# Kernel tuning notes

Hardware: AMD Instinct MI355X
Metric: run time of the kernel (lower is better)

## Reference

```python
import jax, jax.numpy as jnp
import numpy as np

IN_FEATURES = 4096
OUT_FEATURES = 4096
Q_MAX = 127.0  # int8 activation range
EPS = 1e-10


def setup_inputs() -> dict:
    key = jax.random.key(0)
    k1, k2, k3 = jax.random.split(key, 3)
    x = jax.random.normal(k1, (4, 2048, IN_FEATURES), dtype=jnp.float32)
    # Ternary weight in {-1, 0, +1} (the unpacked content of w_packed from pack_tl1).
    w_raw = jax.random.normal(k2, (OUT_FEATURES, IN_FEATURES), dtype=jnp.float32)
    scale = jnp.mean(jnp.abs(w_raw))  # quantize_ternary: scale = |w|.mean()
    w_t = jnp.clip(jnp.round(w_raw / (scale + EPS)), -1.0, 1.0)
    bias = jax.random.normal(k3, (OUT_FEATURES,), dtype=jnp.float32)
    return {"x": x, "w_t": w_t, "w_scale": scale, "bias": bias}


def reference(x, w_t, w_scale, bias):
    """TernaryLinear forward: per-row int8 activation quant, ternary matmul
    with int32 accumulation, scale dequant, bias add.

    x: [..., in], w_t: [out, in] in {-1,0,+1}, w_scale: scalar, bias: [out].
    """
    lead = x.shape[:-1]
    x2 = x.reshape(-1, IN_FEATURES)  # [T, in]
    # Per-row absmax int8 quantization of activations.
    absmax = jnp.max(jnp.abs(x2), axis=-1, keepdims=True)  # [T, 1]
    act_scale = jnp.maximum(absmax, EPS) / Q_MAX
    xq = jnp.clip(jnp.round(x2 / act_scale), -Q_MAX, Q_MAX)  # int-valued [T, in]
    # int32 accumulation (exact in int32; values bounded by 127 * 4096).
    acc = jnp.matmul(xq.astype(jnp.int32), w_t.astype(jnp.int32).T)  # [T, out]
    # Dequantize: y ~= (x @ w_t.T) * w_scale, then bias.
    y = acc.astype(jnp.float32) * act_scale * w_scale + bias
    return y.reshape(*lead, OUT_FEATURES)
```

## Files before the change

kernel.cpp:

```cpp
#include <hip/hip_runtime.h>
#include <stdint.h>

#define T_ROWS 8192
#define IN_F 4096
#define OUT_F 4096

using i32x4 = __attribute__((ext_vector_type(4))) int;
using i32x16 = __attribute__((ext_vector_type(16))) int;

#define GLOBAL_AS __attribute__((address_space(1)))
#define LDS_AS __attribute__((address_space(3)))

static __device__ __forceinline__ void load_lds16(const void* g, void* l) {
    __builtin_amdgcn_global_load_lds((const GLOBAL_AS uint32_t*)g,
                                     (LDS_AS uint32_t*)l, 16, 0, 0);
}

__global__ __launch_bounds__(256) void prep_kernel(const float* __restrict__ x,
                                                   int8_t* __restrict__ xq,
                                                   float* __restrict__ scales,
                                                   const float* __restrict__ w,
                                                   int8_t* __restrict__ w8) {
    if (blockIdx.x < T_ROWS) {
        const int row = blockIdx.x;
        const float* xr = x + (size_t)row * IN_F;
        const float4* xr4 = (const float4*)xr;

        float4 v[4];
        float amax = 0.0f;
#pragma unroll
        for (int i = 0; i < 4; ++i) {
            v[i] = xr4[threadIdx.x + 256 * i];
            amax = fmaxf(amax, fmaxf(fmaxf(fabsf(v[i].x), fabsf(v[i].y)),
                                     fmaxf(fabsf(v[i].z), fabsf(v[i].w))));
        }
#pragma unroll
        for (int off = 32; off; off >>= 1)
            amax = fmaxf(amax, __shfl_xor(amax, off, 64));
        __shared__ float smax[4];
        if ((threadIdx.x & 63) == 0) smax[threadIdx.x >> 6] = amax;
        __syncthreads();
        amax = fmaxf(fmaxf(smax[0], smax[1]), fmaxf(smax[2], smax[3]));

        const float act_scale = fmaxf(amax, 1e-10f) / 127.0f;
        if (threadIdx.x == 0) scales[row] = act_scale;

        int* xqr = (int*)(xq + (size_t)row * IN_F);
#pragma unroll
        for (int i = 0; i < 4; ++i) {
            int q0 = (int)fminf(fmaxf(rintf(v[i].x / act_scale), -127.0f), 127.0f);
            int q1 = (int)fminf(fmaxf(rintf(v[i].y / act_scale), -127.0f), 127.0f);
            int q2 = (int)fminf(fmaxf(rintf(v[i].z / act_scale), -127.0f), 127.0f);
            int q3 = (int)fminf(fmaxf(rintf(v[i].w / act_scale), -127.0f), 127.0f);
            int packed = (q0 & 0xff) | ((q1 & 0xff) << 8) | ((q2 & 0xff) << 16) | (q3 << 24);
            xqr[threadIdx.x + 256 * i] = packed;
        }
    } else {
        const float4* w4 = (const float4*)w;
        int* o4 = (int*)w8;
        size_t base = (size_t)(blockIdx.x - T_ROWS) * 1024 + threadIdx.x;
#pragma unroll
        for (int i = 0; i < 4; ++i) {
            size_t idx = base + 256 * i;
            float4 v = w4[idx];
            int q0 = (int)v.x, q1 = (int)v.y, q2 = (int)v.z, q3 = (int)v.w;
            o4[idx] = (q0 & 0xff) | ((q1 & 0xff) << 8) | ((q2 & 0xff) << 16) | (q3 << 24);
        }
    }
}

__global__ __launch_bounds__(512, 2) void gemm_kernel(const int8_t* __restrict__ xq,
                                                      const int8_t* __restrict__ w8,
                                                      const float* __restrict__ scales,
                                                      const float* __restrict__ bias,
                                                      const float* __restrict__ wscale_p,
                                                      float* __restrict__ out) {
    __shared__ __align__(16) int8_t As[2 * 256 * 128];
    __shared__ __align__(16) int8_t Bs[2 * 256 * 128];

    const int tid = threadIdx.x;
    const int lane = tid & 63;
    const int w = tid >> 6;
    const int wr = w >> 2;
    const int wc = w & 3;
    const int l31 = lane & 31;
    const int lh = lane >> 5;
    const int le = lane & 7;

    int bid = blockIdx.x;
    bid = (bid & 7) * 64 + (bid >> 3);
    const int brow = (bid >> 4) * 256;
    const int bcol = (bid & 15) * 256;

    const int lrow = lane >> 3;
    const int lslot = (lane & 7) ^ lrow;
    const int8_t* srcA = xq + (size_t)(brow + lrow) * IN_F + lslot * 16;
    const int8_t* srcB = w8 + (size_t)(bcol + lrow) * IN_F + lslot * 16;

    const int aBase = (wr * 128 + l31) * 128;
    const int bBase = (wc * 64 + l31) * 128;
    const int slo[4] = { ((0 + lh) ^ le) << 4, ((2 + lh) ^ le) << 4,
                         ((4 + lh) ^ le) << 4, ((6 + lh) ^ le) << 4 };

#define STAGE(LDSA, SRC, BUF, H, KT) do {                                          \
    load_lds16((SRC) + (size_t)((H) * 128 + w * 8) * IN_F + (KT) * 128,            \
               (void*)((LDSA) + (BUF) * 32768 + ((H) * 16 + w) * 1024));           \
    load_lds16((SRC) + (size_t)((H) * 128 + (w + 8) * 8) * IN_F + (KT) * 128,      \
               (void*)((LDSA) + (BUF) * 32768 + ((H) * 16 + w + 8) * 1024));       \
} while (0)

#define PF(FA, FB, BUF, KS) do {                                                   \
    _Pragma("unroll") for (int mi = 0; mi < 4; ++mi)                               \
        FA[mi] = *(const i32x4*)(As + (BUF) * 32768 + aBase + mi * 4096 + slo[KS]);\
    _Pragma("unroll") for (int ni = 0; ni < 2; ++ni)                               \
        FB[ni] = *(const i32x4*)(Bs + (BUF) * 32768 + bBase + ni * 4096 + slo[KS]);\
} while (0)

#define MFMA8(FA, FB) do {                                                         \
    __builtin_amdgcn_s_setprio(1);                                                 \
    _Pragma("unroll") for (int mi = 0; mi < 4; ++mi)                               \
    _Pragma("unroll") for (int ni = 0; ni < 2; ++ni)                               \
        acc[mi][ni] = __builtin_amdgcn_mfma_i32_32x32x32_i8(FA[mi], FB[ni],        \
                                                            acc[mi][ni], 0, 0, 0); \
    __builtin_amdgcn_s_setprio(0);                                                 \
} while (0)

#define BARFENCE do { __builtin_amdgcn_s_barrier(); asm volatile("" ::: "memory"); } while (0)
#define VM0 asm volatile("s_waitcnt vmcnt(0)" ::: "memory")

    i32x16 acc[4][2] = {};
    i32x4 a0[4], b0[2], a1[4], b1[2];

    STAGE(As, srcA, 0, 0, 0);
    STAGE(As, srcA, 0, 1, 0);
    STAGE(Bs, srcB, 0, 0, 0);
    STAGE(Bs, srcB, 0, 1, 0);
    VM0;
    BARFENCE;
    PF(a0, b0, 0, 0);

    for (int t = 0; t < 16; ++t) {
        const int k1 = (2 * t + 1) & 31;
        const int k2 = (2 * t + 2) & 31;
        PF(a1, b1, 0, 1);
        STAGE(As, srcA, 1, 0, k1);
        STAGE(As, srcA, 1, 1, k1);
        STAGE(Bs, srcB, 1, 0, k1);
        MFMA8(a0, b0);
        PF(a0, b0, 0, 2);
        STAGE(Bs, srcB, 1, 1, k1);
        MFMA8(a1, b1);
        PF(a1, b1, 0, 3);
        MFMA8(a0, b0);
        VM0;
        BARFENCE;
        PF(a0, b0, 1, 0);
        MFMA8(a1, b1);
        BARFENCE;
        PF(a1, b1, 1, 1);
        STAGE(As, srcA, 0, 0, k2);
        STAGE(As, srcA, 0, 1, k2);
        STAGE(Bs, srcB, 0, 0, k2);
        MFMA8(a0, b0);
        PF(a0, b0, 1, 2);
        STAGE(Bs, srcB, 0, 1, k2);
        MFMA8(a1, b1);
        PF(a1, b1, 1, 3);
        MFMA8(a0, b0);
        VM0;
        BARFENCE;
        PF(a0, b0, 0, 0);
        MFMA8(a1, b1);
        BARFENCE;
    }

    const float ws = wscale_p[0];
#pragma unroll
    for (int mi = 0; mi < 4; ++mi) {
#pragma unroll
        for (int q = 0; q < 4; ++q) {
#pragma unroll
            for (int r = 0; r < 4; ++r) {
                const int row = brow + wr * 128 + mi * 32 + q * 8 + r + 4 * lh;
                const float sc = scales[row] * ws;
#pragma unroll
                for (int ni = 0; ni < 2; ++ni) {
                    const int col = bcol + wc * 64 + ni * 32 + l31;
                    out[(size_t)row * OUT_F + col] =
                        (float)acc[mi][ni][q * 4 + r] * sc + bias[col];
                }
            }
        }
    }
#undef STAGE
#undef PF
#undef MFMA8
#undef BARFENCE
#undef VM0
}

extern "C" void kernel_launch(void* const* d_in, const int* in_sizes, int n_in,
                              void* d_out, int out_size, void* d_ws, size_t ws_size,
                              hipStream_t stream) {
    const float* x       = (const float*)d_in[0];
    const float* w_t     = (const float*)d_in[1];
    const float* w_scale = (const float*)d_in[2];
    const float* bias    = (const float*)d_in[3];
    float* out = (float*)d_out;

    int8_t* xq     = (int8_t*)d_ws;
    float*  scales = (float*)((char*)d_ws + (size_t)T_ROWS * IN_F);
    int8_t* w8     = (int8_t*)((char*)d_ws + (size_t)T_ROWS * IN_F + T_ROWS * sizeof(float));

    prep_kernel<<<T_ROWS + (OUT_F * IN_F) / (16 * 256), 256, 0, stream>>>(
        x, xq, scales, w_t, w8);

    gemm_kernel<<<(T_ROWS / 256) * (OUT_F / 256), 512, 0, stream>>>(
        xq, w8, scales, bias, w_scale, out);
}
```

Baseline: 192.5 us.

## Add extra LDS swizzle bit and pin LDS-load/MFMA overlap with sched barriers

```diff
diff --git a/kernel.cpp b/kernel.cpp
--- a/kernel.cpp
+++ b/kernel.cpp
@@ -93,7 +93,7 @@
     const int bcol = (bid & 15) * 256;
 
     const int lrow = lane >> 3;
-    const int lslot = (lane & 7) ^ lrow;
+    const int lslot = (lane & 7) ^ lrow ^ (((w >> 2) & 1) << 2);
     const int8_t* srcA = xq + (size_t)(brow + lrow) * IN_F + lslot * 16;
     const int8_t* srcB = w8 + (size_t)(bcol + lrow) * IN_F + lslot * 16;
 
@@ -111,9 +111,11 @@
 
 #define PF(FA, FB, BUF, KS) do {                                                   \
     _Pragma("unroll") for (int mi = 0; mi < 4; ++mi)                               \
-        FA[mi] = *(const i32x4*)(As + (BUF) * 32768 + aBase + mi * 4096 + slo[KS]);\
+        FA[mi] = *(const i32x4*)(As + (BUF) * 32768 + aBase + mi * 4096 +          \
+                                 (slo[KS] ^ ((mi & 1) << 6)));                     \
     _Pragma("unroll") for (int ni = 0; ni < 2; ++ni)                               \
-        FB[ni] = *(const i32x4*)(Bs + (BUF) * 32768 + bBase + ni * 4096 + slo[KS]);\
+        FB[ni] = *(const i32x4*)(Bs + (BUF) * 32768 + bBase + ni * 4096 +          \
+                                 (slo[KS] ^ ((ni & 1) << 6)));                     \
 } while (0)
 
 #define MFMA8(FA, FB) do {                                                         \
@@ -125,6 +127,16 @@
     __builtin_amdgcn_s_setprio(0);                                                 \
 } while (0)
 
+#define PHASE(PFS, STAGES, FA, FB) do {                                            \
+    PFS;                                                                           \
+    STAGES;                                                                        \
+    __builtin_amdgcn_sched_barrier(0);                                             \
+    asm volatile("s_waitcnt lgkmcnt(6)" ::: "memory");                             \
+    __builtin_amdgcn_sched_barrier(0);                                             \
+    MFMA8(FA, FB);                                                                 \
+    __builtin_amdgcn_sched_barrier(0);                                             \
+} while (0)
+
 #define BARFENCE do { __builtin_amdgcn_s_barrier(); asm volatile("" ::: "memory"); } while (0)
 #define VM0 asm volatile("s_waitcnt vmcnt(0)" ::: "memory")
 
@@ -142,35 +154,25 @@
     for (int t = 0; t < 16; ++t) {
         const int k1 = (2 * t + 1) & 31;
         const int k2 = (2 * t + 2) & 31;
-        PF(a1, b1, 0, 1);
-        STAGE(As, srcA, 1, 0, k1);
-        STAGE(As, srcA, 1, 1, k1);
-        STAGE(Bs, srcB, 1, 0, k1);
-        MFMA8(a0, b0);
-        PF(a0, b0, 0, 2);
-        STAGE(Bs, srcB, 1, 1, k1);
-        MFMA8(a1, b1);
-        PF(a1, b1, 0, 3);
-        MFMA8(a0, b0);
+        PHASE(PF(a1, b1, 0, 1),
+              STAGE(As, srcA, 1, 0, k1); STAGE(As, srcA, 1, 1, k1);
+              STAGE(Bs, srcB, 1, 0, k1),
+              a0, b0);
+        PHASE(PF(a0, b0, 0, 2), STAGE(Bs, srcB, 1, 1, k1), a1, b1);
+        PHASE(PF(a1, b1, 0, 3), , a0, b0);
         VM0;
         BARFENCE;
-        PF(a0, b0, 1, 0);
-        MFMA8(a1, b1);
-        BARFENCE;
-        PF(a1, b1, 1, 1);
-        STAGE(As, srcA, 0, 0, k2);
-        STAGE(As, srcA, 0, 1, k2);
-        STAGE(Bs, srcB, 0, 0, k2);
-        MFMA8(a0, b0);
-        PF(a0, b0, 1, 2);
-        STAGE(Bs, srcB, 0, 1, k2);
-        MFMA8(a1, b1);
-        PF(a1, b1, 1, 3);
-        MFMA8(a0, b0);
+        PHASE(PF(a0, b0, 1, 0), , a1, b1);
+        BARFENCE;
+        PHASE(PF(a1, b1, 1, 1),
+              STAGE(As, srcA, 0, 0, k2); STAGE(As, srcA, 0, 1, k2);
+              STAGE(Bs, srcB, 0, 0, k2),
+              a0, b0);
+        PHASE(PF(a0, b0, 1, 2), STAGE(Bs, srcB, 0, 1, k2), a1, b1);
+        PHASE(PF(a1, b1, 1, 3), , a0, b0);
         VM0;
         BARFENCE;
-        PF(a0, b0, 0, 0);
-        MFMA8(a1, b1);
+        PHASE(PF(a0, b0, 0, 0), , a1, b1);
         BARFENCE;
     }
 
@@ -195,6 +197,7 @@
 #undef STAGE
 #undef PF
 #undef MFMA8
+#undef PHASE
 #undef BARFENCE
 #undef VM0
 }
```

After: 191.7 us. About the same (-0.4%).
